# Kernel tuning notes

Measured on AMD Instinct MI355X. Metric: run time of the kernel, lower is better.

Reference implementation:

```python
import jax, jax.numpy as jnp
import numpy as np

D_MODEL = 1024
NUM_HEADS = 16
HEAD_DIM = D_MODEL // NUM_HEADS
B, S = 2, 2048


def setup_inputs() -> dict:
    key = jax.random.key(0)
    ks = jax.random.split(key, 7)
    scale = 1.0 / np.sqrt(D_MODEL)
    return {
        "query": jax.random.normal(ks[0], (B, S, D_MODEL), jnp.float32),
        "key": jax.random.normal(ks[1], (B, S, D_MODEL), jnp.float32),
        "value": jax.random.normal(ks[2], (B, S, D_MODEL), jnp.float32),
        "Wq": jax.random.normal(ks[3], (D_MODEL, D_MODEL), jnp.float32) * scale,
        "Wk": jax.random.normal(ks[4], (D_MODEL, D_MODEL), jnp.float32) * scale,
        "Wv": jax.random.normal(ks[5], (D_MODEL, D_MODEL), jnp.float32) * scale,
        "Wo": jax.random.normal(ks[6], (D_MODEL, D_MODEL), jnp.float32) * scale,
    }


def reference(query, key, value, Wq, Wk, Wv, Wo):
    b, tl, _ = query.shape
    sl = key.shape[1]
    # Linear (no bias): x @ W.T, then split heads -> (B, H, L, Dh)
    def split_heads(x, L):
        return x.reshape(b, L, NUM_HEADS, HEAD_DIM).transpose(0, 2, 1, 3)
    Q = split_heads(query @ Wq.T, tl)
    K = split_heads(key @ Wk.T, sl)
    V = split_heads(value @ Wv.T, sl)
    scores = jnp.einsum("bhqd,bhkd->bhqk", Q, K) / jnp.sqrt(jnp.float32(HEAD_DIM))
    attn_weights = jax.nn.softmax(scores, axis=-1)
    # dropout is identity in eval mode
    context = jnp.einsum("bhqk,bhkd->bhqd", attn_weights, V)
    context = context.transpose(0, 2, 1, 3).reshape(b, tl, D_MODEL)
    output = context @ Wo.T
    return (output, attn_weights)
```

## Files before the change

kernel.cpp:

```cpp
#include <hip/hip_runtime.h>
#include <stdint.h>
#include <stddef.h>

#define D_MODEL 1024
#define NHEADS  16
#define HDIM    64
#define BB      2
#define SSEQ    2048

using bf16x8 = __attribute__((ext_vector_type(8))) short;
using f32x4  = __attribute__((ext_vector_type(4))) float;
using s16x4  = __attribute__((ext_vector_type(4))) short;

static __device__ __forceinline__ float b2f(short s) {
  union { float f; unsigned u; } v;
  v.u = ((unsigned)(unsigned short)s) << 16;
  return v.f;
}
static __device__ __forceinline__ short f2b(float f) {
  union { float f; unsigned u; } v;
  v.f = f;
  unsigned r = v.u + 0x7fffu + ((v.u >> 16) & 1u);
  return (short)(r >> 16);
}

static __device__ __forceinline__ void gload16(const void* g, void* l) {
  __builtin_amdgcn_global_load_lds(
      (const __attribute__((address_space(1))) unsigned int*)g,
      (__attribute__((address_space(3))) unsigned int*)l, 16, 0, 0);
}

__global__ __launch_bounds__(256) void k_cvt(const float* __restrict__ src,
                                             short* __restrict__ dst, int n4) {
  int i = blockIdx.x * blockDim.x + threadIdx.x;
  const int stride = gridDim.x * blockDim.x;
  for (; i < n4; i += stride) {
    const float4 v = ((const float4*)src)[i];
    s16x4 o;
    o[0] = f2b(v.x); o[1] = f2b(v.y); o[2] = f2b(v.z); o[3] = f2b(v.w);
    ((s16x4*)dst)[i] = o;
  }
}

template <bool F32OUT>
static __device__ __forceinline__ void gemm_bt_dev(
    const short* __restrict__ A, const short* __restrict__ W, void* __restrict__ Cv,
    int N, int K) {
  __shared__ short sA[128 * 32];
  __shared__ short sB[128 * 32];

  const int t  = threadIdx.x;
  const int l  = t & 63;
  const int w  = t >> 6;
  const int wm = w >> 1, wn = w & 1;
  const int g  = l >> 4, lr = l & 15;
  const int m0 = blockIdx.y * 128;
  const int n0 = blockIdx.x * 128;

  f32x4 acc[4][4];
#pragma unroll
  for (int i = 0; i < 4; ++i)
#pragma unroll
    for (int j = 0; j < 4; ++j) {
      acc[i][j][0] = 0.f; acc[i][j][1] = 0.f;
      acc[i][j][2] = 0.f; acc[i][j][3] = 0.f;
    }

  const int r0 = t >> 2;
  const int c0 = (t & 3) * 8;
  const short* ga0 = A + (size_t)(m0 + r0) * K + c0;
  const short* ga1 = A + (size_t)(m0 + 64 + r0) * K + c0;
  const short* gb0 = W + (size_t)(n0 + r0) * K + c0;
  const short* gb1 = W + (size_t)(n0 + 64 + r0) * K + c0;
  short* la0 = &sA[(t & ~63) * 8];
  short* la1 = la0 + 256 * 8;
  short* lb0 = &sB[(t & ~63) * 8];
  short* lb1 = lb0 + 256 * 8;

  for (int k0 = 0; k0 < K; k0 += 32) {
    __syncthreads();
    gload16(ga0 + k0, la0);
    gload16(ga1 + k0, la1);
    gload16(gb0 + k0, lb0);
    gload16(gb1 + k0, lb1);
    __syncthreads();

    bf16x8 af[4], bfr[4];
#pragma unroll
    for (int i = 0; i < 4; ++i)
      af[i] = *(const bf16x8*)&sA[(wm * 64 + i * 16 + lr) * 32 + g * 8];
#pragma unroll
    for (int i = 0; i < 4; ++i)
      bfr[i] = *(const bf16x8*)&sB[(wn * 64 + i * 16 + lr) * 32 + g * 8];
#pragma unroll
    for (int i = 0; i < 4; ++i)
#pragma unroll
      for (int j = 0; j < 4; ++j)
        acc[i][j] = __builtin_amdgcn_mfma_f32_16x16x32_bf16(af[i], bfr[j],
                                                            acc[i][j], 0, 0, 0);
  }

#pragma unroll
  for (int i = 0; i < 4; ++i)
#pragma unroll
    for (int j = 0; j < 4; ++j)
#pragma unroll
      for (int rr = 0; rr < 4; ++rr) {
        const int row = m0 + wm * 64 + i * 16 + g * 4 + rr;
        const int col = n0 + wn * 64 + j * 16 + lr;
        if (F32OUT)
          ((float*)Cv)[(size_t)row * N + col] = acc[i][j][rr];
        else
          ((short*)Cv)[(size_t)row * N + col] = f2b(acc[i][j][rr]);
      }
}

__global__ __launch_bounds__(256) void k_gemm_f32out(
    const short* __restrict__ A, const short* __restrict__ W,
    float* __restrict__ C, int N, int K) {
  gemm_bt_dev<true>(A, W, C, N, K);
}

__global__ __launch_bounds__(256) void k_gemm_qkv(
    const short* __restrict__ q, const short* __restrict__ k,
    const short* __restrict__ v, const short* __restrict__ wq,
    const short* __restrict__ wk, const short* __restrict__ wv,
    short* __restrict__ Qb, short* __restrict__ Kb, short* __restrict__ Vb) {
  const short *A, *W;
  short* C;
  if (blockIdx.z == 0)      { A = q; W = wq; C = Qb; }
  else if (blockIdx.z == 1) { A = k; W = wk; C = Kb; }
  else                      { A = v; W = wv; C = Vb; }
  gemm_bt_dev<false>(A, W, C, D_MODEL, D_MODEL);
}

__global__ __launch_bounds__(256) void k_transpose_v(
    const short* __restrict__ Vb, short* __restrict__ Vt) {
  __shared__ short tile[64][66];
  const int bh = blockIdx.x;
  const int b = bh >> 4, h = bh & 15;
  const int s0 = blockIdx.y * 64;
  const int t = threadIdx.x;
#pragma unroll
  for (int i = 0; i < 16; ++i) {
    int e = t + i * 256;
    int si = e >> 6, dj = e & 63;
    tile[si][dj] = Vb[((size_t)b * SSEQ + s0 + si) * D_MODEL + h * HDIM + dj];
  }
  __syncthreads();
#pragma unroll
  for (int i = 0; i < 16; ++i) {
    int e = t + i * 256;
    int dj = e >> 6, si = e & 63;
    Vt[((size_t)bh * HDIM + dj) * SSEQ + s0 + si] = tile[si][dj];
  }
}

__global__ __launch_bounds__(256) void k_attn(
    const short* __restrict__ Qb, const short* __restrict__ Kb,
    const short* __restrict__ Vt, float* __restrict__ attnO,
    short* __restrict__ ctx) {
  __shared__ short S[16 * SSEQ];
  const int t = threadIdx.x;
  const int l = t & 63, w = t >> 6;
  const int g = l >> 4, lr = l & 15;
  const int bh = blockIdx.y;
  const int b = bh >> 4, h = bh & 15;
  const int q0 = blockIdx.x * 16;

  const size_t qoff = ((size_t)b * SSEQ + q0 + lr) * D_MODEL + h * HDIM;
  const bf16x8 aq0 = *(const bf16x8*)&Qb[qoff + g * 8];
  const bf16x8 aq1 = *(const bf16x8*)&Qb[qoff + 32 + g * 8];

  const short* Kh = Kb + (size_t)b * SSEQ * D_MODEL + h * HDIM;

  for (int nt = 0; nt < 32; ++nt) {
    const int n0 = (w * 32 + nt) * 16;
    const short* krow = Kh + (size_t)(n0 + lr) * D_MODEL;
    const bf16x8 bk0 = *(const bf16x8*)&krow[g * 8];
    const bf16x8 bk1 = *(const bf16x8*)&krow[32 + g * 8];
    f32x4 acc;
    acc[0] = 0.f; acc[1] = 0.f; acc[2] = 0.f; acc[3] = 0.f;
    acc = __builtin_amdgcn_mfma_f32_16x16x32_bf16(aq0, bk0, acc, 0, 0, 0);
    acc = __builtin_amdgcn_mfma_f32_16x16x32_bf16(aq1, bk1, acc, 0, 0, 0);
#pragma unroll
    for (int rr = 0; rr < 4; ++rr) {
      const int row = g * 4 + rr;
      const int col = n0 + lr;
      const int pc = (col >> 3) ^ (row & 7);
      S[row * SSEQ + pc * 8 + (col & 7)] = f2b(acc[rr] * 0.125f);
    }
  }
  __syncthreads();

  const int r = t >> 4, j = t & 15;
  float mx = -1e30f;
  for (int i = 0; i < 16; ++i) {
    const int c = j + (i << 4);
    const int pc = c ^ (r & 7);
    const bf16x8 v = *(const bf16x8*)&S[r * SSEQ + pc * 8];
#pragma unroll
    for (int e = 0; e < 8; ++e) mx = fmaxf(mx, b2f(v[e]));
  }
#pragma unroll
  for (int mask = 1; mask < 16; mask <<= 1)
    mx = fmaxf(mx, __shfl_xor(mx, mask, 64));

  float sum = 0.f;
  for (int i = 0; i < 16; ++i) {
    const int c = j + (i << 4);
    const int pc = c ^ (r & 7);
    const bf16x8 v = *(const bf16x8*)&S[r * SSEQ + pc * 8];
#pragma unroll
    for (int e = 0; e < 8; ++e) sum += __expf(b2f(v[e]) - mx);
  }
#pragma unroll
  for (int mask = 1; mask < 16; mask <<= 1) sum += __shfl_xor(sum, mask, 64);
  const float inv = 1.f / sum;

  float* arow = attnO + ((size_t)bh * SSEQ + q0 + r) * SSEQ;
  for (int i = 0; i < 16; ++i) {
    const int c = j + (i << 4);
    const int pc = c ^ (r & 7);
    const bf16x8 v = *(const bf16x8*)&S[r * SSEQ + pc * 8];
    bf16x8 p;
#pragma unroll
    for (int e = 0; e < 8; ++e) {
      const float pe = __expf(b2f(v[e]) - mx) * inv;
      p[e] = f2b(pe);
      arow[(size_t)c * 8 + e] = pe;
    }
    *(bf16x8*)&S[r * SSEQ + pc * 8] = p;
  }
  __syncthreads();

  const short* Vh = Vt + (size_t)bh * HDIM * SSEQ;
  const int d0 = w * 16;
  f32x4 acc;
  acc[0] = 0.f; acc[1] = 0.f; acc[2] = 0.f; acc[3] = 0.f;
  for (int s0 = 0; s0 < SSEQ; s0 += 32) {
    const int pc = ((s0 >> 3) + g) ^ (lr & 7);
    const bf16x8 ap = *(const bf16x8*)&S[lr * SSEQ + pc * 8];
    const bf16x8 bv =
        *(const bf16x8*)&Vh[(size_t)(d0 + lr) * SSEQ + s0 + g * 8];
    acc = __builtin_amdgcn_mfma_f32_16x16x32_bf16(ap, bv, acc, 0, 0, 0);
  }
#pragma unroll
  for (int rr = 0; rr < 4; ++rr) {
    const int qr = q0 + g * 4 + rr;
    ctx[((size_t)b * SSEQ + qr) * D_MODEL + h * HDIM + d0 + lr] =
        f2b(acc[rr]);
  }
}

extern "C" void kernel_launch(void* const* d_in, const int* in_sizes, int n_in,
                              void* d_out, int out_size, void* d_ws,
                              size_t ws_size, hipStream_t stream) {
  const float* qf  = (const float*)d_in[0];
  const float* kf  = (const float*)d_in[1];
  const float* vf  = (const float*)d_in[2];
  const float* wqf = (const float*)d_in[3];
  const float* wkf = (const float*)d_in[4];
  const float* wvf = (const float*)d_in[5];
  const float* wof = (const float*)d_in[6];

  float* out  = (float*)d_out;
  float* attn = out + (size_t)BB * SSEQ * D_MODEL;

  const size_t NTOK = (size_t)BB * SSEQ;
  const size_t XN = NTOK * D_MODEL;
  const size_t WN = (size_t)D_MODEL * D_MODEL;

  short* qb  = (short*)d_ws;
  short* kb  = qb + XN;
  short* vb  = kb + XN;
  short* wqb = vb + XN;
  short* wkb = wqb + WN;
  short* wvb = wkb + WN;
  short* wob = wvb + WN;
  short* Qb  = wob + WN;
  short* Kb  = Qb + XN;
  short* Vb  = Kb + XN;
  short* Vt  = Vb + XN;
  short* ctx = Vt + XN;

  k_cvt<<<512, 256, 0, stream>>>(qf, qb, (int)(XN / 4));
  k_cvt<<<512, 256, 0, stream>>>(kf, kb, (int)(XN / 4));
  k_cvt<<<512, 256, 0, stream>>>(vf, vb, (int)(XN / 4));
  k_cvt<<<256, 256, 0, stream>>>(wqf, wqb, (int)(WN / 4));
  k_cvt<<<256, 256, 0, stream>>>(wkf, wkb, (int)(WN / 4));
  k_cvt<<<256, 256, 0, stream>>>(wvf, wvb, (int)(WN / 4));
  k_cvt<<<256, 256, 0, stream>>>(wof, wob, (int)(WN / 4));

  k_gemm_qkv<<<dim3(D_MODEL / 128, NTOK / 128, 3), 256, 0, stream>>>(
      qb, kb, vb, wqb, wkb, wvb, Qb, Kb, Vb);
  k_transpose_v<<<dim3(BB * NHEADS, SSEQ / 64), 256, 0, stream>>>(Vb, Vt);
  k_attn<<<dim3(SSEQ / 16, BB * NHEADS), 256, 0, stream>>>(Qb, Kb, Vt, attn,
                                                           ctx);
  k_gemm_f32out<<<dim3(D_MODEL / 128, NTOK / 128), 256, 0, stream>>>(
      ctx, wob, out, D_MODEL, D_MODEL);
}
```

Measured before the change: 907.0 us.

## Restructure attention into two-pass online softmax with split-K per wave

Replaces the 64KB shared-memory score buffer with a two-pass scheme: the first pass computes running max and sum per row using online softmax, and the second recomputes QK^T, writes the normalized probabilities, and accumulates PV through a small per-wave tile. Each wave handles a quarter of the keys for all 64 head dims, and partial outputs are reduced through shared memory at the end. The launch becomes a 1D grid with a remapped block index so that neighbouring blocks share a head. LDS drops sharply, which should raise occupancy, at the cost of computing QK^T twice and reading K twice.

After: 956.0 us. +5.4%, slower.

```diff
diff --git a/kernel.cpp b/kernel.cpp
--- a/kernel.cpp
+++ b/kernel.cpp
@@ -160,96 +160,149 @@
     const short* __restrict__ Qb, const short* __restrict__ Kb,
     const short* __restrict__ Vt, float* __restrict__ attnO,
     short* __restrict__ ctx) {
-  __shared__ short S[16 * SSEQ];
+  __shared__ __attribute__((aligned(16))) short ptile[4][16][40];
+  __shared__ float wmx[4][16];
+  __shared__ float wls[4][16];
+  __shared__ f32x4 red[4][4][64];
+
   const int t = threadIdx.x;
   const int l = t & 63, w = t >> 6;
   const int g = l >> 4, lr = l & 15;
-  const int bh = blockIdx.y;
+  const int orig = blockIdx.x;
+  const int id = (orig & 7) * 512 + (orig >> 3);
+  const int q0 = (id & 127) * 16;
+  const int bh = id >> 7;
   const int b = bh >> 4, h = bh & 15;
-  const int q0 = blockIdx.x * 16;
 
   const size_t qoff = ((size_t)b * SSEQ + q0 + lr) * D_MODEL + h * HDIM;
   const bf16x8 aq0 = *(const bf16x8*)&Qb[qoff + g * 8];
   const bf16x8 aq1 = *(const bf16x8*)&Qb[qoff + 32 + g * 8];
 
   const short* Kh = Kb + (size_t)b * SSEQ * D_MODEL + h * HDIM;
-
-  for (int nt = 0; nt < 32; ++nt) {
-    const int n0 = (w * 32 + nt) * 16;
-    const short* krow = Kh + (size_t)(n0 + lr) * D_MODEL;
-    const bf16x8 bk0 = *(const bf16x8*)&krow[g * 8];
-    const bf16x8 bk1 = *(const bf16x8*)&krow[32 + g * 8];
-    f32x4 acc;
-    acc[0] = 0.f; acc[1] = 0.f; acc[2] = 0.f; acc[3] = 0.f;
-    acc = __builtin_amdgcn_mfma_f32_16x16x32_bf16(aq0, bk0, acc, 0, 0, 0);
-    acc = __builtin_amdgcn_mfma_f32_16x16x32_bf16(aq1, bk1, acc, 0, 0, 0);
+  const short* Vh = Vt + (size_t)bh * HDIM * SSEQ;
+  const int kbase = w * 512;
+
+  float pm[4], pl[4];
+#pragma unroll
+  for (int rr = 0; rr < 4; ++rr) { pm[rr] = -1e30f; pl[rr] = 0.f; }
+
+  for (int st = 0; st < 16; ++st) {
+    const int n0 = kbase + st * 32;
+    const short* kr0 = Kh + (size_t)(n0 + lr) * D_MODEL;
+    const short* kr1 = Kh + (size_t)(n0 + 16 + lr) * D_MODEL;
+    const bf16x8 ka0 = *(const bf16x8*)&kr0[g * 8];
+    const bf16x8 ka1 = *(const bf16x8*)&kr0[32 + g * 8];
+    const bf16x8 kb0 = *(const bf16x8*)&kr1[g * 8];
+    const bf16x8 kb1 = *(const bf16x8*)&kr1[32 + g * 8];
+    f32x4 sA, sB;
+    sA[0] = 0.f; sA[1] = 0.f; sA[2] = 0.f; sA[3] = 0.f;
+    sB[0] = 0.f; sB[1] = 0.f; sB[2] = 0.f; sB[3] = 0.f;
+    sA = __builtin_amdgcn_mfma_f32_16x16x32_bf16(aq0, ka0, sA, 0, 0, 0);
+    sA = __builtin_amdgcn_mfma_f32_16x16x32_bf16(aq1, ka1, sA, 0, 0, 0);
+    sB = __builtin_amdgcn_mfma_f32_16x16x32_bf16(aq0, kb0, sB, 0, 0, 0);
+    sB = __builtin_amdgcn_mfma_f32_16x16x32_bf16(aq1, kb1, sB, 0, 0, 0);
+#pragma unroll
+    for (int rr = 0; rr < 4; ++rr) {
+      const float s1 = sA[rr] * 0.125f;
+      const float s2 = sB[rr] * 0.125f;
+      const float nm = fmaxf(pm[rr], fmaxf(s1, s2));
+      pl[rr] = pl[rr] * __expf(pm[rr] - nm) + __expf(s1 - nm) + __expf(s2 - nm);
+      pm[rr] = nm;
+    }
+  }
+#pragma unroll
+  for (int mask = 1; mask < 16; mask <<= 1) {
+#pragma unroll
+    for (int rr = 0; rr < 4; ++rr) {
+      const float om = __shfl_xor(pm[rr], mask, 64);
+      const float ol = __shfl_xor(pl[rr], mask, 64);
+      const float nm = fmaxf(pm[rr], om);
+      pl[rr] = pl[rr] * __expf(pm[rr] - nm) + ol * __expf(om - nm);
+      pm[rr] = nm;
+    }
+  }
+  if (lr == 0) {
+#pragma unroll
+    for (int rr = 0; rr < 4; ++rr) {
+      wmx[w][g * 4 + rr] = pm[rr];
+      wls[w][g * 4 + rr] = pl[rr];
+    }
+  }
+  __syncthreads();
+
+  float M[4], inv[4];
+#pragma unroll
+  for (int rr = 0; rr < 4; ++rr) {
+    const int row = g * 4 + rr;
+    const float m0 = wmx[0][row], m1 = wmx[1][row];
+    const float m2 = wmx[2][row], m3 = wmx[3][row];
+    const float Mv = fmaxf(fmaxf(m0, m1), fmaxf(m2, m3));
+    const float L = wls[0][row] * __expf(m0 - Mv) + wls[1][row] * __expf(m1 - Mv) +
+                    wls[2][row] * __expf(m2 - Mv) + wls[3][row] * __expf(m3 - Mv);
+    M[rr] = Mv;
+    inv[rr] = 1.f / L;
+  }
+
+  f32x4 accO[4];
+#pragma unroll
+  for (int u = 0; u < 4; ++u) {
+    accO[u][0] = 0.f; accO[u][1] = 0.f; accO[u][2] = 0.f; accO[u][3] = 0.f;
+  }
+  float* arow0 = attnO + ((size_t)bh * SSEQ + q0) * SSEQ;
+
+  for (int st = 0; st < 16; ++st) {
+    const int n0 = kbase + st * 32;
+    const short* kr0 = Kh + (size_t)(n0 + lr) * D_MODEL;
+    const short* kr1 = Kh + (size_t)(n0 + 16 + lr) * D_MODEL;
+    const bf16x8 ka0 = *(const bf16x8*)&kr0[g * 8];
+    const bf16x8 ka1 = *(const bf16x8*)&kr0[32 + g * 8];
+    const bf16x8 kb0 = *(const bf16x8*)&kr1[g * 8];
+    const bf16x8 kb1 = *(const bf16x8*)&kr1[32 + g * 8];
+    bf16x8 bv[4];
+#pragma unroll
+    for (int u = 0; u < 4; ++u)
+      bv[u] = *(const bf16x8*)&Vh[(size_t)(u * 16 + lr) * SSEQ + n0 + g * 8];
+
+    f32x4 sA, sB;
+    sA[0] = 0.f; sA[1] = 0.f; sA[2] = 0.f; sA[3] = 0.f;
+    sB[0] = 0.f; sB[1] = 0.f; sB[2] = 0.f; sB[3] = 0.f;
+    sA = __builtin_amdgcn_mfma_f32_16x16x32_bf16(aq0, ka0, sA, 0, 0, 0);
+    sA = __builtin_amdgcn_mfma_f32_16x16x32_bf16(aq1, ka1, sA, 0, 0, 0);
+    sB = __builtin_amdgcn_mfma_f32_16x16x32_bf16(aq0, kb0, sB, 0, 0, 0);
+    sB = __builtin_amdgcn_mfma_f32_16x16x32_bf16(aq1, kb1, sB, 0, 0, 0);
+
 #pragma unroll
     for (int rr = 0; rr < 4; ++rr) {
       const int row = g * 4 + rr;
-      const int col = n0 + lr;
-      const int pc = (col >> 3) ^ (row & 7);
-      S[row * SSEQ + pc * 8 + (col & 7)] = f2b(acc[rr] * 0.125f);
-    }
-  }
+      const float pa = __expf(sA[rr] * 0.125f - M[rr]) * inv[rr];
+      const float pb = __expf(sB[rr] * 0.125f - M[rr]) * inv[rr];
+      arow0[(size_t)row * SSEQ + n0 + lr] = pa;
+      arow0[(size_t)row * SSEQ + n0 + 16 + lr] = pb;
+      ptile[w][row][lr] = f2b(pa);
+      ptile[w][row][16 + lr] = f2b(pb);
+    }
+    const bf16x8 ap = *(const bf16x8*)&ptile[w][lr][g * 8];
+#pragma unroll
+    for (int u = 0; u < 4; ++u)
+      accO[u] = __builtin_amdgcn_mfma_f32_16x16x32_bf16(ap, bv[u], accO[u], 0, 0, 0);
+  }
+
+#pragma unroll
+  for (int u = 0; u < 4; ++u) red[w][u][l] = accO[u];
   __syncthreads();
-
-  const int r = t >> 4, j = t & 15;
-  float mx = -1e30f;
-  for (int i = 0; i < 16; ++i) {
-    const int c = j + (i << 4);
-    const int pc = c ^ (r & 7);
-    const bf16x8 v = *(const bf16x8*)&S[r * SSEQ + pc * 8];
-#pragma unroll
-    for (int e = 0; e < 8; ++e) mx = fmaxf(mx, b2f(v[e]));
-  }
-#pragma unroll
-  for (int mask = 1; mask < 16; mask <<= 1)
-    mx = fmaxf(mx, __shfl_xor(mx, mask, 64));
-
-  float sum = 0.f;
-  for (int i = 0; i < 16; ++i) {
-    const int c = j + (i << 4);
-    const int pc = c ^ (r & 7);
-    const bf16x8 v = *(const bf16x8*)&S[r * SSEQ + pc * 8];
-#pragma unroll
-    for (int e = 0; e < 8; ++e) sum += __expf(b2f(v[e]) - mx);
-  }
-#pragma unroll
-  for (int mask = 1; mask < 16; mask <<= 1) sum += __shfl_xor(sum, mask, 64);
-  const float inv = 1.f / sum;
-
-  float* arow = attnO + ((size_t)bh * SSEQ + q0 + r) * SSEQ;
-  for (int i = 0; i < 16; ++i) {
-    const int c = j + (i << 4);
-    const int pc = c ^ (r & 7);
-    const bf16x8 v = *(const bf16x8*)&S[r * SSEQ + pc * 8];
-    bf16x8 p;
-#pragma unroll
-    for (int e = 0; e < 8; ++e) {
-      const float pe = __expf(b2f(v[e]) - mx) * inv;
-      p[e] = f2b(pe);
-      arow[(size_t)c * 8 + e] = pe;
-    }
-    *(bf16x8*)&S[r * SSEQ + pc * 8] = p;
-  }
-  __syncthreads();
-
-  const short* Vh = Vt + (size_t)bh * HDIM * SSEQ;
-  const int d0 = w * 16;
-  f32x4 acc;
-  acc[0] = 0.f; acc[1] = 0.f; acc[2] = 0.f; acc[3] = 0.f;
-  for (int s0 = 0; s0 < SSEQ; s0 += 32) {
-    const int pc = ((s0 >> 3) + g) ^ (lr & 7);
-    const bf16x8 ap = *(const bf16x8*)&S[lr * SSEQ + pc * 8];
-    const bf16x8 bv =
-        *(const bf16x8*)&Vh[(size_t)(d0 + lr) * SSEQ + s0 + g * 8];
-    acc = __builtin_amdgcn_mfma_f32_16x16x32_bf16(ap, bv, acc, 0, 0, 0);
-  }
-#pragma unroll
-  for (int rr = 0; rr < 4; ++rr) {
-    const int qr = q0 + g * 4 + rr;
-    ctx[((size_t)b * SSEQ + qr) * D_MODEL + h * HDIM + d0 + lr] =
-        f2b(acc[rr]);
+  {
+    f32x4 o = red[0][w][l];
+    const f32x4 o1 = red[1][w][l], o2 = red[2][w][l], o3 = red[3][w][l];
+    o[0] += o1[0] + o2[0] + o3[0];
+    o[1] += o1[1] + o2[1] + o3[1];
+    o[2] += o1[2] + o2[2] + o3[2];
+    o[3] += o1[3] + o2[3] + o3[3];
+#pragma unroll
+    for (int rr = 0; rr < 4; ++rr) {
+      const int qr = q0 + g * 4 + rr;
+      ctx[((size_t)b * SSEQ + qr) * D_MODEL + h * HDIM + w * 16 + lr] =
+          f2b(o[rr]);
+    }
   }
 }
 
@@ -295,8 +348,7 @@
   k_gemm_qkv<<<dim3(D_MODEL / 128, NTOK / 128, 3), 256, 0, stream>>>(
       qb, kb, vb, wqb, wkb, wvb, Qb, Kb, Vb);
   k_transpose_v<<<dim3(BB * NHEADS, SSEQ / 64), 256, 0, stream>>>(Vb, Vt);
-  k_attn<<<dim3(SSEQ / 16, BB * NHEADS), 256, 0, stream>>>(Qb, Kb, Vt, attn,
-                                                           ctx);
+  k_attn<<<4096, 256, 0, stream>>>(Qb, Kb, Vt, attn, ctx);
   k_gemm_f32out<<<dim3(D_MODEL / 128, NTOK / 128), 256, 0, stream>>>(
       ctx, wob, out, D_MODEL, D_MODEL);
 }
```
